# Kernel optimization log

Measured on AMD Instinct MI355X. Metric: run time of the kernel, lower is better.

Reference implementation:

```python
import jax, jax.numpy as jnp
import numpy as np

S, I, IN_DIM, PROJ_DIM, OUT_DIM = 128, 384, 256, 32, 128
LN_EPS = 1e-5


def _layer_norm(x):
    # utils.normalize in OmegaFold: F.layer_norm over last dim, no affine params
    mu = jnp.mean(x, axis=-1, keepdims=True)
    var = jnp.var(x, axis=-1, keepdims=True)
    return (x - mu) * jax.lax.rsqrt(var + LN_EPS)


def setup_inputs() -> dict:
    key = jax.random.key(0)
    k0, k1, k2, k3 = jax.random.split(key, 4)
    node_repr = jax.random.normal(k0, (S, I, IN_DIM), dtype=jnp.float32)
    mask = (jax.random.uniform(k1, (S, I)) < 0.9).astype(jnp.float32)
    W_proj = jax.random.normal(k2, (IN_DIM, 2 * PROJ_DIM), dtype=jnp.float32) / np.sqrt(IN_DIM)
    b_proj = jnp.zeros((2 * PROJ_DIM,), dtype=jnp.float32)
    out_weights = jax.random.normal(k3, (PROJ_DIM, PROJ_DIM, OUT_DIM), dtype=jnp.float32) * 0.02
    out_bias = jnp.zeros((OUT_DIM,), dtype=jnp.float32)
    return {
        "node_repr": node_repr,
        "mask": mask,
        "W_proj": W_proj,
        "b_proj": b_proj,
        "out_weights": out_weights,
        "out_bias": out_bias,
    }


def reference(node_repr, mask, W_proj, b_proj, out_weights, out_bias):
    # LayerNorm (no affine) -> linear projection to 2*proj_dim
    x = _layer_norm(node_repr)                       # [s, i, in_dim]
    act = x @ W_proj + b_proj                        # [s, i, 2d]
    m = mask[..., None]                              # [s, i, 1]
    act = act * m
    # mask-pair counts: einsum('si,sj->ij')
    norm = jnp.einsum("si,sj->ij", mask, mask)[..., None]  # [i, j, 1]
    l = act[..., :PROJ_DIM]                          # [s, i, d]
    r = act[..., PROJ_DIM:]                          # [s, j, e]
    # outer-product mean over s, then contract (d,e)->f with the 3-tensor
    outer = jnp.einsum("sid,sje->ijde", l, r)        # [i, j, d, e]
    out = jnp.einsum("ijde,def->ijf", outer, out_weights) + out_bias  # [i, j, f]
    return out / (norm + 0.001)
```

## Files before the change

### kernel.cpp

```cpp
#include <hip/hip_runtime.h>

#define S_DIM 128
#define I_DIM 384
#define IN_DIM 256
#define PD 32
#define ODIM 128

typedef __attribute__((ext_vector_type(8))) __bf16 bf16x8;
typedef __attribute__((ext_vector_type(4))) float f32x4;

#define MFMA16(a, b, c) __builtin_amdgcn_mfma_f32_16x16x32_bf16((a), (b), (c), 0, 0, 0)

__device__ inline unsigned short f2bf(float f) {
    unsigned int u = __builtin_bit_cast(unsigned int, f);
    unsigned int r = (u + 0x7FFFu + ((u >> 16) & 1u)) >> 16;
    return (unsigned short)r;
}

__global__ void prep_cast(const float* __restrict__ Wp, const float* __restrict__ W2,
                          unsigned short* __restrict__ WpT, unsigned short* __restrict__ W2s) {
    int t = blockIdx.x * 256 + threadIdx.x;
    if (t < 64 * 256) {
        int f = t >> 8, k = t & 255;
        WpT[t] = f2bf(Wp[k * 64 + f]);
    }
    if (t < 128 * 1024) {
        int e = t >> 12;
        int f = (t >> 5) & 127;
        int d = t & 31;
        W2s[t] = f2bf(W2[(d * 32 + e) * 128 + f]);
    }
}

__global__ void norm_kernel(const float* __restrict__ mask, float* __restrict__ invn) {
    __shared__ float mi[S_DIM][16];
    __shared__ float mj[S_DIM][16];
    int t = threadIdx.x;
    int i0 = blockIdx.y * 16, j0 = blockIdx.x * 16;
    for (int p = 0; p < 8; ++p) {
        int s = p * 16 + (t >> 4);
        int c = t & 15;
        mi[s][c] = mask[s * I_DIM + i0 + c];
        mj[s][c] = mask[s * I_DIM + j0 + c];
    }
    __syncthreads();
    int ii = t >> 4, jj = t & 15;
    float acc = 0.f;
#pragma unroll 8
    for (int s = 0; s < S_DIM; ++s) acc += mi[s][ii] * mj[s][jj];
    invn[(i0 + ii) * I_DIM + (j0 + jj)] = 1.0f / (acc + 0.001f);
}

__global__ __launch_bounds__(256, 4) void ln_proj(const float* __restrict__ x,
                                                  const float* __restrict__ mask,
                                                  const float* __restrict__ bias,
                                                  const unsigned short* __restrict__ WpT_g,
                                                  unsigned short* __restrict__ lT,
                                                  unsigned short* __restrict__ rT) {
    __shared__ unsigned short xsh[64 * 264];
    int t = threadIdx.x;
    int w = t >> 6, lane = t & 63;
    int i = blockIdx.x >> 1;
    int s0 = (blockIdx.x & 1) * 64;

    float4 vbuf[4];
#pragma unroll
    for (int p = 0; p < 4; ++p)
        vbuf[p] = *(const float4*)(x + ((size_t)(s0 + w * 16 + p) * I_DIM + i) * IN_DIM + lane * 4);

    for (int it = 0; it < 16; ++it) {
        float4 v = vbuf[it & 3];
        if (it + 4 < 16)
            vbuf[it & 3] = *(const float4*)(x + ((size_t)(s0 + w * 16 + it + 4) * I_DIM + i) * IN_DIM + lane * 4);
        float s1 = v.x + v.y + v.z + v.w;
        float s2 = v.x * v.x + v.y * v.y + v.z * v.z + v.w * v.w;
#pragma unroll
        for (int off = 32; off >= 1; off >>= 1) {
            s1 += __shfl_xor(s1, off);
            s2 += __shfl_xor(s2, off);
        }
        float mu = s1 * (1.f / 256.f);
        float var = s2 * (1.f / 256.f) - mu * mu;
        float rs = rsqrtf(var + 1e-5f);
        unsigned int h0 = f2bf((v.x - mu) * rs);
        unsigned int h1 = f2bf((v.y - mu) * rs);
        unsigned int h2 = f2bf((v.z - mu) * rs);
        unsigned int h3 = f2bf((v.w - mu) * rs);
        uint2 pk;
        pk.x = h0 | (h1 << 16);
        pk.y = h2 | (h3 << 16);
        *(uint2*)&xsh[(w * 16 + it) * 264 + lane * 4] = pk;
    }
    __syncthreads();

    int l15 = lane & 15, q = lane >> 4;
    f32x4 acc[4];
#pragma unroll
    for (int nt = 0; nt < 4; ++nt) acc[nt] = (f32x4){0.f, 0.f, 0.f, 0.f};

    for (int k0 = 0; k0 < 256; k0 += 32) {
        bf16x8 a = *(bf16x8*)&xsh[(w * 16 + l15) * 264 + k0 + q * 8];
#pragma unroll
        for (int nt = 0; nt < 4; ++nt) {
            bf16x8 b = *(const bf16x8*)&WpT_g[(nt * 16 + l15) * 256 + k0 + q * 8];
            acc[nt] = MFMA16(a, b, acc[nt]);
        }
    }

    float mval[4];
#pragma unroll
    for (int reg = 0; reg < 4; ++reg)
        mval[reg] = mask[(size_t)(s0 + w * 16 + q * 4 + reg) * I_DIM + i];

    __syncthreads();
    unsigned short* trsh = xsh;

#pragma unroll
    for (int nt = 0; nt < 4; ++nt) {
        int f = nt * 16 + l15;
        float bv = bias[f];
        unsigned int lo = (unsigned int)f2bf((acc[nt][0] + bv) * mval[0]) |
                          ((unsigned int)f2bf((acc[nt][1] + bv) * mval[1]) << 16);
        unsigned int hi = (unsigned int)f2bf((acc[nt][2] + bv) * mval[2]) |
                          ((unsigned int)f2bf((acc[nt][3] + bv) * mval[3]) << 16);
        uint2 pk; pk.x = lo; pk.y = hi;
        *(uint2*)&trsh[f * 72 + w * 16 + q * 4] = pk;
    }
    __syncthreads();

    {
        int fr = t >> 2, so = (t & 3) * 16;
        unsigned short* dst = ((fr < 32) ? lT : rT) + ((size_t)(i * 32 + (fr & 31)) * 128 + s0 + so);
        *(uint4*)dst = *(uint4*)&trsh[fr * 72 + so];
        *(uint4*)(dst + 8) = *(uint4*)&trsh[fr * 72 + so + 8];
    }
}

__global__ __launch_bounds__(512, 4) void fused_kernel(const unsigned short* __restrict__ lT,
                                                       const unsigned short* __restrict__ rT,
                                                       const unsigned short* __restrict__ W2s,
                                                       const float* __restrict__ invn,
                                                       const float* __restrict__ out_bias,
                                                       float* __restrict__ out) {
    __shared__ unsigned short sh[32768];
    __shared__ unsigned short w2b[8192];
    char* shb = (char*)sh;
    int t = threadIdx.x;
    int w = t >> 6, lane = t & 63, l15 = lane & 15, q = lane >> 4;
    int bx = blockIdx.x;
    int by = blockIdx.y;
    int wm = w >> 1, wn = w & 1;

    {
        int row = t >> 2, c0 = (t & 3) * 32;
        const unsigned short* rbase = rT + (size_t)(bx * 128 + row) * 128 + c0;
        uint4 v0 = ((const uint4*)rbase)[0];
        uint4 v1 = ((const uint4*)rbase)[1];
        uint4 v2 = ((const uint4*)rbase)[2];
        uint4 v3 = ((const uint4*)rbase)[3];
        *(uint4*)&sh[row * 136 + c0] = v0;
        *(uint4*)&sh[row * 136 + c0 + 8] = v1;
        *(uint4*)&sh[row * 136 + c0 + 16] = v2;
        *(uint4*)&sh[row * 136 + c0 + 24] = v3;
    }

    const unsigned short* lbase = lT + (size_t)(by * 256 + wm * 64 + l15) * 128 + q * 8;
    bf16x8 a0_ = *(const bf16x8*)(lbase);
    bf16x8 a1_ = *(const bf16x8*)(lbase + 2048);
    bf16x8 a2_ = *(const bf16x8*)(lbase + 4096);
    bf16x8 a3_ = *(const bf16x8*)(lbase + 6144);
    __syncthreads();

    f32x4 acc[4][4];
#pragma unroll
    for (int mt = 0; mt < 4; ++mt)
#pragma unroll
        for (int nt = 0; nt < 4; ++nt) acc[mt][nt] = (f32x4){0.f, 0.f, 0.f, 0.f};

#pragma unroll
    for (int k0 = 0; k0 < 4; ++k0) {
        bf16x8 a[4];
        if (k0 == 0) {
            a[0] = a0_; a[1] = a1_; a[2] = a2_; a[3] = a3_;
        } else {
#pragma unroll
            for (int mt = 0; mt < 4; ++mt)
                a[mt] = *(const bf16x8*)(lbase + mt * 2048 + k0 * 32);
        }
#pragma unroll
        for (int nt = 0; nt < 4; ++nt) {
            bf16x8 b = *(bf16x8*)&sh[(wn * 64 + nt * 16 + l15) * 136 + k0 * 32 + q * 8];
#pragma unroll
            for (int mt = 0; mt < 4; ++mt)
                acc[mt][nt] = MFMA16(a[mt], b, acc[mt][nt]);
        }
    }
    __syncthreads();

#define DMA_W2(K0_)                                                                     \
    __builtin_amdgcn_global_load_lds(                                                   \
        (const __attribute__((address_space(1))) unsigned int*)(const void*)(W2s + (K0_) * 4096 + t * 8), \
        (__attribute__((address_space(3))) unsigned int*)(void*)(&w2b[((K0_) & 1) * 4096 + w * 512]),     \
        16, 0, 0)

    DMA_W2(0);
    DMA_W2(1);

#pragma unroll
    for (int mt = 0; mt < 4; ++mt) {
        int i_loc = wm * 2 + (mt >> 1);
        int dbase2 = ((mt & 1) * 16 + q * 4) * 2;
#pragma unroll
        for (int nt = 0; nt < 4; ++nt) {
            int pair = i_loc * 4 + wn * 2 + (nt >> 1);
            int e = (nt & 1) * 16 + l15;
            unsigned int lo = (unsigned int)f2bf(acc[mt][nt][0]) | ((unsigned int)f2bf(acc[mt][nt][1]) << 16);
            unsigned int hi = (unsigned int)f2bf(acc[mt][nt][2]) | ((unsigned int)f2bf(acc[mt][nt][3]) << 16);
            uint2 pk; pk.x = lo; pk.y = hi;
            *(uint2*)(shb + pair * 2048 + ((e * 64 + dbase2) ^ ((e & 7) << 4) ^ ((pair & 7) << 4))) = pk;
        }
    }
    __syncthreads();

    f32x4 acc3[2];
    acc3[0] = (f32x4){0.f, 0.f, 0.f, 0.f};
    acc3[1] = (f32x4){0.f, 0.f, 0.f, 0.f};
    char* gbase0 = shb + l15 * 2048;
    char* gbase1 = shb + (16 + l15) * 2048;
    int sx = (l15 & 7) << 4;
    int brow = (w * 16 + l15) * 32 + q * 8;

#pragma unroll 2
    for (int k0 = 0; k0 < 31; ++k0) {
        asm volatile("s_waitcnt vmcnt(1)" ::: "memory");
        bf16x8 b = *(bf16x8*)&w2b[(k0 & 1) * 4096 + brow];
        int off = ((k0 * 64 + q * 16) ^ ((k0 & 7) << 4)) ^ sx;
        bf16x8 a0 = *(bf16x8*)(gbase0 + off);
        bf16x8 a1 = *(bf16x8*)(gbase1 + off);
        asm volatile("s_waitcnt lgkmcnt(0)" ::: "memory");
        if (k0 < 30) { DMA_W2(k0 + 2); }
        __builtin_amdgcn_sched_barrier(0);
        __builtin_amdgcn_s_setprio(1);
        acc3[0] = MFMA16(a0, b, acc3[0]);
        acc3[1] = MFMA16(a1, b, acc3[1]);
        __builtin_amdgcn_s_setprio(0);
    }
    {
        asm volatile("s_waitcnt vmcnt(0)" ::: "memory");
        bf16x8 b = *(bf16x8*)&w2b[(31 & 1) * 4096 + brow];
        int off = ((31 * 64 + q * 16) ^ ((31 & 7) << 4)) ^ sx;
        bf16x8 a0 = *(bf16x8*)(gbase0 + off);
        bf16x8 a1 = *(bf16x8*)(gbase1 + off);
        acc3[0] = MFMA16(a0, b, acc3[0]);
        acc3[1] = MFMA16(a1, b, acc3[1]);
    }
#undef DMA_W2

    float bv = out_bias[w * 16 + l15];
#pragma unroll
    for (int mt3 = 0; mt3 < 2; ++mt3) {
#pragma unroll
        for (int reg = 0; reg < 4; ++reg) {
            int pair = mt3 * 16 + q * 4 + reg;
            int gi = by * 8 + (pair >> 2);
            int gj = bx * 4 + (pair & 3);
            float vinv = invn[gi * I_DIM + gj];
            out[((size_t)gi * I_DIM + gj) * 128 + w * 16 + l15] = (acc3[mt3][reg] + bv) * vinv;
        }
    }
}

extern "C" void kernel_launch(void* const* d_in, const int* in_sizes, int n_in,
                              void* d_out, int out_size, void* d_ws, size_t ws_size,
                              hipStream_t stream) {
    const float* node = (const float*)d_in[0];
    const float* mask = (const float*)d_in[1];
    const float* Wp   = (const float*)d_in[2];
    const float* bp   = (const float*)d_in[3];
    const float* W2   = (const float*)d_in[4];
    const float* bo   = (const float*)d_in[5];
    float* out = (float*)d_out;

    char* ws = (char*)d_ws;
    unsigned short* lT  = (unsigned short*)(ws);
    unsigned short* rT  = (unsigned short*)(ws + 3145728);
    unsigned short* W2s = (unsigned short*)(ws + 6291456);
    unsigned short* WpT = (unsigned short*)(ws + 6553600);
    float*          inv = (float*)(ws + 6586368);

    hipLaunchKernelGGL(prep_cast, dim3(512), dim3(256), 0, stream, Wp, W2, WpT, W2s);
    hipLaunchKernelGGL(norm_kernel, dim3(24, 24), dim3(256), 0, stream, mask, inv);
    hipLaunchKernelGGL(ln_proj, dim3(768), dim3(256), 0, stream, node, mask, bp, WpT, lT, rT);
    hipLaunchKernelGGL(fused_kernel, dim3(96, 48), dim3(512), 0, stream,
                       lT, rT, W2s, inv, bo, out);
}
```

Baseline: 269.3 us.

## Software-pipeline LDS fragment loads in W2 contraction and swizzle block order

The second-stage contraction loop now double-buffers its LDS operand fragments in registers, loading step k+1 while the MFMAs for step k run. The loop is fully unrolled and the sched_barrier is removed. Block indices are also remapped with an interleaving swizzle over the 96-wide grid, which changes which tiles run concurrently and so their L2 reuse. The aim is to hide LDS latency and improve cache locality, at the cost of higher register pressure and longer code. The buffer reuse around the DMA_W2 waits also needs careful ordering to stay correct.

```diff
diff --git a/kernel.cpp b/kernel.cpp
--- a/kernel.cpp
+++ b/kernel.cpp
@@ -147,8 +147,11 @@
     char* shb = (char*)sh;
     int t = threadIdx.x;
     int w = t >> 6, lane = t & 63, l15 = lane & 15, q = lane >> 4;
-    int bx = blockIdx.x;
-    int by = blockIdx.y;
+
+    int lin = blockIdx.y * 96 + blockIdx.x;
+    int nlin = (lin & 7) * 576 + (lin >> 3);
+    int bx = nlin % 96;
+    int by = nlin / 96;
     int wm = w >> 1, wn = w & 1;
 
     {
@@ -230,29 +233,40 @@
     int sx = (l15 & 7) << 4;
     int brow = (w * 16 + l15) * 32 + q * 8;
 
-#pragma unroll 2
-    for (int k0 = 0; k0 < 31; ++k0) {
+    bf16x8 bfr[2], af0[2], af1[2];
+    {
+        int off0 = (0 ^ (q * 16)) ^ sx;
+        bfr[0] = *(bf16x8*)&w2b[brow];
+        af0[0] = *(bf16x8*)(gbase0 + off0);
+        af1[0] = *(bf16x8*)(gbase1 + off0);
+    }
+
+#pragma unroll
+    for (int k0 = 0; k0 < 30; ++k0) {
+        asm volatile("s_waitcnt lgkmcnt(0)" ::: "memory");
+        DMA_W2(k0 + 2);
         asm volatile("s_waitcnt vmcnt(1)" ::: "memory");
-        bf16x8 b = *(bf16x8*)&w2b[(k0 & 1) * 4096 + brow];
-        int off = ((k0 * 64 + q * 16) ^ ((k0 & 7) << 4)) ^ sx;
-        bf16x8 a0 = *(bf16x8*)(gbase0 + off);
-        bf16x8 a1 = *(bf16x8*)(gbase1 + off);
-        asm volatile("s_waitcnt lgkmcnt(0)" ::: "memory");
-        if (k0 < 30) { DMA_W2(k0 + 2); }
-        __builtin_amdgcn_sched_barrier(0);
+        int offn = (((k0 + 1) * 64 + q * 16) ^ (((k0 + 1) & 7) << 4)) ^ sx;
+        bfr[(k0 + 1) & 1] = *(bf16x8*)&w2b[((k0 + 1) & 1) * 4096 + brow];
+        af0[(k0 + 1) & 1] = *(bf16x8*)(gbase0 + offn);
+        af1[(k0 + 1) & 1] = *(bf16x8*)(gbase1 + offn);
         __builtin_amdgcn_s_setprio(1);
-        acc3[0] = MFMA16(a0, b, acc3[0]);
-        acc3[1] = MFMA16(a1, b, acc3[1]);
+        acc3[0] = MFMA16(af0[k0 & 1], bfr[k0 & 1], acc3[0]);
+        acc3[1] = MFMA16(af1[k0 & 1], bfr[k0 & 1], acc3[1]);
         __builtin_amdgcn_s_setprio(0);
     }
     {
         asm volatile("s_waitcnt vmcnt(0)" ::: "memory");
-        bf16x8 b = *(bf16x8*)&w2b[(31 & 1) * 4096 + brow];
-        int off = ((31 * 64 + q * 16) ^ ((31 & 7) << 4)) ^ sx;
-        bf16x8 a0 = *(bf16x8*)(gbase0 + off);
-        bf16x8 a1 = *(bf16x8*)(gbase1 + off);
-        acc3[0] = MFMA16(a0, b, acc3[0]);
-        acc3[1] = MFMA16(a1, b, acc3[1]);
+        int off31 = ((31 * 64 + q * 16) ^ ((31 & 7) << 4)) ^ sx;
+        bfr[1] = *(bf16x8*)&w2b[1 * 4096 + brow];
+        af0[1] = *(bf16x8*)(gbase0 + off31);
+        af1[1] = *(bf16x8*)(gbase1 + off31);
+        acc3[0] = MFMA16(af0[0], bfr[0], acc3[0]);
+        acc3[1] = MFMA16(af1[0], bfr[0], acc3[1]);
+    }
+    {
+        acc3[0] = MFMA16(af0[1], bfr[1], acc3[0]);
+        acc3[1] = MFMA16(af1[1], bfr[1], acc3[1]);
     }
 #undef DMA_W2
 
```

New measurement: 281.9 us. +4.7%, slower.
